# Optimization experiments

Measured on AMD Instinct MI355X. Metric: run time of the kernel, lower is better.

The kernel has to match this reference:

```python
import jax, jax.numpy as jnp
import numpy as np
from jax import lax

DN = ('NCHW', 'OIHW', 'NCHW')
BETA = 0.25


def _conv(x, w, b, stride, pad):
    y = lax.conv_general_dilated(x, w, (stride, stride), [(pad, pad), (pad, pad)],
                                 dimension_numbers=DN)
    return y + b[None, :, None, None]


def _convT(x, w, b, stride, pad, opad):
    # torch ConvTranspose2d(w: [in,out,kh,kw]) == dilated conv with flipped, transposed kernel
    k = w.shape[2]
    wf = jnp.transpose(w, (1, 0, 2, 3))[:, :, ::-1, ::-1]
    lo = k - 1 - pad
    hi = k - 1 - pad + opad
    y = lax.conv_general_dilated(x, wf, (1, 1), [(lo, hi), (lo, hi)],
                                 lhs_dilation=(stride, stride), dimension_numbers=DN)
    return y + b[None, :, None, None]


def setup_inputs() -> dict:
    key = jax.random.key(0)
    ks = jax.random.split(key, 16)
    s = 0.05
    inp = {
        'x': jax.random.normal(ks[0], (64, 3, 125, 125), jnp.float32),
        'enc_w1': jax.random.normal(ks[1], (32, 3, 3, 3), jnp.float32) * s,
        'enc_b1': jnp.zeros((32,), jnp.float32),
        'enc_w2': jax.random.normal(ks[2], (64, 32, 3, 3), jnp.float32) * s,
        'enc_b2': jnp.zeros((64,), jnp.float32),
        'enc_w3': jax.random.normal(ks[3], (64, 64, 1, 1), jnp.float32) * s,
        'enc_b3': jnp.zeros((64,), jnp.float32),
        'codebook': jax.random.normal(ks[4], (512, 64), jnp.float32),
        'dec_w1': jax.random.normal(ks[5], (64, 64, 3, 3), jnp.float32) * s,  # torch [in,out,kh,kw]
        'dec_b1': jnp.zeros((64,), jnp.float32),
        'dec_w2': jax.random.normal(ks[6], (64, 32, 3, 3), jnp.float32) * s,
        'dec_b2': jnp.zeros((32,), jnp.float32),
        'dec_w3': jax.random.normal(ks[7], (32, 3, 2, 2), jnp.float32) * s,
        'dec_b3': jnp.zeros((3,), jnp.float32),
    }
    return inp


def reference(x, enc_w1, enc_b1, enc_w2, enc_b2, enc_w3, enc_b3, codebook,
              dec_w1, dec_b1, dec_w2, dec_b2, dec_w3, dec_b3):
    # Encoder
    z = jax.nn.relu(_conv(x, enc_w1, enc_b1, 2, 1))
    z = jax.nn.relu(_conv(z, enc_w2, enc_b2, 2, 1))
    z = _conv(z, enc_w3, enc_b3, 1, 0)  # [B, D, h, w]

    # VQ (training mode)
    zp = jnp.transpose(z, (0, 2, 3, 1))  # [B, h, w, D]
    flat = zp.reshape(-1, zp.shape[-1])  # [N, D]
    d = (jnp.sum(flat * flat, axis=1, keepdims=True)
         + jnp.sum(codebook * codebook, axis=1)
         - 2.0 * flat @ codebook.T)  # [N, K]
    idx = jnp.argmin(d, axis=1)
    q = codebook[idx].reshape(zp.shape)

    q_latent_loss = jnp.mean((q - lax.stop_gradient(zp)) ** 2)
    e_latent_loss = jnp.mean((zp - lax.stop_gradient(q)) ** 2)
    e_q_loss = q_latent_loss + BETA * e_latent_loss

    q_st = zp + lax.stop_gradient(q - zp)  # straight-through
    e = jnp.transpose(q_st, (0, 3, 1, 2))

    # Decoder
    h = jax.nn.relu(_convT(e, dec_w1, dec_b1, 2, 1, 1))
    h = jax.nn.relu(_convT(h, dec_w2, dec_b2, 2, 1, 1))
    x_recon = _convT(h, dec_w3, dec_b3, 1, 2, 0)

    recon_loss = jnp.sum((x_recon - x) ** 2)
    loss_sum = e_q_loss + recon_loss
    return (loss_sum, e_q_loss, recon_loss, x_recon)
```

## Files before the change

kernel.cpp:

```cpp
#include <hip/hip_runtime.h>

#define DEV __device__ __forceinline__
typedef unsigned short u16;
typedef __bf16 bf16x8 __attribute__((ext_vector_type(8)));
typedef float f32x4 __attribute__((ext_vector_type(4)));

DEV u16 f2bf(float f) {
  unsigned u = __float_as_uint(f);
  u += 0x7FFF + ((u >> 16) & 1);
  return (u16)(u >> 16);
}


__global__ __launch_bounds__(256) void k_prep(
    const float* __restrict__ ew1, const float* __restrict__ ew2,
    const float* __restrict__ ew3, const float* __restrict__ dw1,
    const float* __restrict__ dw2, const float* __restrict__ dw3,
    const float* __restrict__ cb,
    float* __restrict__ wc1p, float* __restrict__ wc3p,
    u16* __restrict__ w3f, float* __restrict__ c2,
    u16* __restrict__ w2f, u16* __restrict__ wt1f, u16* __restrict__ wt2f,
    u16* __restrict__ cbf) {
  int i = blockIdx.x * 256 + threadIdx.x;
  if (i < 864) {
    int cl = i & 7; int t = i >> 3; int tap = t % 9; t /= 9; int ci = t % 3; int cog = t / 3;
    wc1p[i] = ew1[((cog * 8 + cl) * 3 + ci) * 9 + tap];
  } else if (i < 4960) {
    int j = i - 864; int cl = j & 7; int t = j >> 3; int ci = t & 63; int cog = t >> 6;
    wc3p[j] = ew3[(cog * 8 + cl) * 64 + ci];
  } else if (i < 9056) {
    int j = i - 4960;
    int jj = j & 7; int lane = (j >> 3) & 63; int tp = (j >> 9) & 3; int hl = j >> 11;
    int kh = tp >> 1, kw = tp & 1;
    int ci = ((lane >> 4) << 3) + jj; int co = lane & 15;
    float wv = (co < 3) ? dw3[((ci * 3 + co) * 2 + kh) * 2 + kw] : 0.f;
    u16 hi = f2bf(wv);
    if (hl == 0) w3f[j] = hi;
    else         w3f[j] = f2bf(wv - __uint_as_float((unsigned)hi << 16));
  } else if (i < 9568) {
    int k = i - 9056;
    const float4* c4 = (const float4*)(cb + (k << 6));
    float s = 0.f;
    #pragma unroll
    for (int q = 0; q < 16; ++q) { float4 v = c4[q]; s += v.x*v.x + v.y*v.y + v.z*v.z + v.w*v.w; }
    c2[k] = s;
  } else if (i < 28000) {
    int j = i - 9568;
    int jj = j & 7; int lane = (j >> 3) & 63; int nf = (j >> 9) & 3; int kt = j >> 11;
    int kh = kt / 3, kw = kt % 3;
    int ci = ((lane >> 4) << 3) + jj; int co = (nf << 4) + (lane & 15);
    w2f[j] = f2bf(ew2[((co * 32 + ci) * 3 + kh) * 3 + kw]);
  } else if (i < 64864) {
    int j = i - 28000;
    int jj = j & 7; int lane = (j >> 3) & 63; int nf = (j >> 9) & 3; int s = (j >> 11) & 1; int kt = j >> 12;
    int kh = kt / 3, kw = kt % 3;
    int ci = (s << 5) + ((lane >> 4) << 3) + jj; int co = (nf << 4) + (lane & 15);
    wt1f[j] = f2bf(dw1[((ci * 64 + co) * 3 + kh) * 3 + kw]);
  } else if (i < 83296) {
    int j = i - 64864;
    int jj = j & 7; int lane = (j >> 3) & 63; int nf = (j >> 9) & 1; int s = (j >> 10) & 1; int kt = j >> 11;
    int kh = kt / 3, kw = kt % 3;
    int ci = (s << 5) + ((lane >> 4) << 3) + jj; int co = (nf << 4) + (lane & 15);
    wt2f[j] = f2bf(dw2[((ci * 32 + co) * 3 + kh) * 3 + kw]);
  } else if (i < 148832) {
    int j = i - 83296;
    int jj = j & 7; int lane = (j >> 3) & 63; int nt = (j >> 9) & 31; int ks = (j >> 14) & 1; int hl = j >> 15;
    int ci = (ks << 5) + ((lane >> 4) << 3) + jj;
    int code = (nt << 4) + (lane & 15);
    float v = cb[(code << 6) + ci];
    u16 hi = f2bf(v);
    cbf[j] = hl ? f2bf(v - __uint_as_float((unsigned)hi << 16)) : hi;
  }
}

__global__ __launch_bounds__(256) void k_pad(
    const float* __restrict__ x, float* __restrict__ xp) {
  int idx = blockIdx.x * 256 + threadIdx.x;
  int c4 = idx & 31;
  int r  = (idx >> 5) % 129;
  int cbp = (idx >> 5) / 129;
  int ih = r - 1;
  float4 v = make_float4(0.f, 0.f, 0.f, 0.f);
  if ((unsigned)ih < 125u) {
    const float* rp = x + (cbp * 125 + ih) * 125;
    int iw0 = c4 * 4 - 1;
    if (iw0 >= 0)        v.x = rp[iw0];
    if (iw0 + 1 < 125)   v.y = rp[iw0 + 1];
    if (iw0 + 2 < 125)   v.z = rp[iw0 + 2];
    if (iw0 + 3 < 125)   v.w = rp[iw0 + 3];
  }
  *(float4*)(xp + (cbp * 129 + r) * 128 + c4 * 4) = v;
}

__global__ __launch_bounds__(256) void k_conv1(
    const float* __restrict__ xp, const float* __restrict__ wp,
    const float* __restrict__ bias, u16* __restrict__ z1t) {
  __shared__ u16 st[256 * 34];
  int t = threadIdx.x;
  int slab = blockIdx.x & 15, b = blockIdx.x >> 4;
  int tx = t & 15, ty = (t >> 4) & 3, cg = t >> 6;
  int oh = slab * 4 + ty;
  int co0 = cg * 8;
  const float* wcg = wp + cg * 216;
  float acc[8][4];
  #pragma unroll
  for (int c = 0; c < 8; ++c) {
    float bv = bias[co0 + c];
    #pragma unroll
    for (int s = 0; s < 4; ++s) acc[c][s] = bv;
  }
  #pragma unroll
  for (int ci = 0; ci < 3; ++ci) {
    #pragma unroll
    for (int kh = 0; kh < 3; ++kh) {
      const float* rp = xp + ((b * 3 + ci) * 129 + (2 * oh + kh)) * 128 + 8 * tx;
      float4 qa = *(const float4*)rp;
      float4 qb = *(const float4*)(rp + 4);
      float v8 = rp[8];
      float v[9] = {qa.x, qa.y, qa.z, qa.w, qb.x, qb.y, qb.z, qb.w, v8};
      #pragma unroll
      for (int kw = 0; kw < 3; ++kw) {
        const float* wq = wcg + (ci * 9 + kh * 3 + kw) * 8;
        float4 wa = *(const float4*)wq;
        float4 wb = *(const float4*)(wq + 4);
        float w8[8] = {wa.x, wa.y, wa.z, wa.w, wb.x, wb.y, wb.z, wb.w};
        #pragma unroll
        for (int s = 0; s < 4; ++s) {
          float in = v[2 * s + kw];
          #pragma unroll
          for (int c = 0; c < 8; ++c) acc[c][s] = fmaf(in, w8[c], acc[c][s]);
        }
      }
    }
  }
  #pragma unroll
  for (int s = 0; s < 4; ++s) {
    bool wok = (tx * 4 + s) < 63;
    unsigned p0 = 0, p1 = 0, p2 = 0, p3 = 0;
    if (wok) {
      p0 = f2bf(fmaxf(acc[0][s], 0.f)) | ((unsigned)f2bf(fmaxf(acc[1][s], 0.f)) << 16);
      p1 = f2bf(fmaxf(acc[2][s], 0.f)) | ((unsigned)f2bf(fmaxf(acc[3][s], 0.f)) << 16);
      p2 = f2bf(fmaxf(acc[4][s], 0.f)) | ((unsigned)f2bf(fmaxf(acc[5][s], 0.f)) << 16);
      p3 = f2bf(fmaxf(acc[6][s], 0.f)) | ((unsigned)f2bf(fmaxf(acc[7][s], 0.f)) << 16);
    }
    int lpix = tx * 16 + ty * 4 + s;
    *(uint4*)&st[lpix * 34 + co0] = make_uint4(p0, p1, p2, p3);
// ... 145 lines not shown
    #pragma unroll
    for (int r = 0; r < 4; ++r) { bs[mt][r] = 3.4e38f; bix[mt][r] = 0; }
  for (int nt = 0; nt < 32; ++nt) {
    const u16* bp = cbf + lane * 8;
    bf16x8 Bh0 = *(const bf16x8*)(bp + (nt << 9));
    bf16x8 Bh1 = *(const bf16x8*)(bp + ((32 + nt) << 9));
    bf16x8 Bl0 = *(const bf16x8*)(bp + ((64 + nt) << 9));
    bf16x8 Bl1 = *(const bf16x8*)(bp + ((96 + nt) << 9));
    float c2 = c2v[(nt << 4) + n];
    #pragma unroll
    for (int mt = 0; mt < 4; ++mt) {
      f32x4 acc = {0.f, 0.f, 0.f, 0.f};
      acc = __builtin_amdgcn_mfma_f32_16x16x32_bf16(Ah[mt][0], Bh0, acc, 0, 0, 0);
      acc = __builtin_amdgcn_mfma_f32_16x16x32_bf16(Ah[mt][1], Bh1, acc, 0, 0, 0);
      acc = __builtin_amdgcn_mfma_f32_16x16x32_bf16(Al[mt][0], Bh0, acc, 0, 0, 0);
      acc = __builtin_amdgcn_mfma_f32_16x16x32_bf16(Al[mt][1], Bh1, acc, 0, 0, 0);
      acc = __builtin_amdgcn_mfma_f32_16x16x32_bf16(Ah[mt][0], Bl0, acc, 0, 0, 0);
      acc = __builtin_amdgcn_mfma_f32_16x16x32_bf16(Ah[mt][1], Bl1, acc, 0, 0, 0);
      int idx = (nt << 4) + n;
      #pragma unroll
      for (int r = 0; r < 4; ++r) {
        float sc = fmaf(-2.f, acc[r], c2);
        if (sc < bs[mt][r]) { bs[mt][r] = sc; bix[mt][r] = idx; }
      }
    }
  }
  #pragma unroll
  for (int off = 8; off > 0; off >>= 1) {
    #pragma unroll
    for (int mt = 0; mt < 4; ++mt)
      #pragma unroll
      for (int r = 0; r < 4; ++r) {
        float os = __shfl_xor(bs[mt][r], off, 16);
        int oi = __shfl_xor(bix[mt][r], off, 16);
        if (os < bs[mt][r] || (os == bs[mt][r] && oi < bix[mt][r])) {
          bs[mt][r] = os; bix[mt][r] = oi;
        }
      }
  }
  if (n == 0) {
    #pragma unroll
    for (int mt = 0; mt < 4; ++mt)
      #pragma unroll
      for (int r = 0; r < 4; ++r)
        idxb[p0 + mt * 16 + q * 4 + r] = bix[mt][r];
  }
}

__global__ __launch_bounds__(256) void k_vqf(
    const float* __restrict__ z3, const float* __restrict__ cb,
    const int* __restrict__ idxb, u16* __restrict__ et,
    float* __restrict__ acc) {
  int n = blockIdx.x * 256 + threadIdx.x;
  int bi = idxb[n];
  int b = n >> 10, hw = n & 1023;
  const float* zp = z3 + (b << 16) + hw;
  uint2* ep = (uint2*)(et + (n << 6));
  const float4* cq = (const float4*)(cb + (bi << 6));
  float lsum = 0.f;
  #pragma unroll
  for (int i = 0; i < 16; ++i) {
    float4 c = cq[i];
    float zv, df;
    zv = zp[(4*i+0) << 10]; df = c.x - zv; lsum = fmaf(df, df, lsum);
    zv = zp[(4*i+1) << 10]; df = c.y - zv; lsum = fmaf(df, df, lsum);
    zv = zp[(4*i+2) << 10]; df = c.z - zv; lsum = fmaf(df, df, lsum);
    zv = zp[(4*i+3) << 10]; df = c.w - zv; lsum = fmaf(df, df, lsum);
    ep[i] = make_uint2(f2bf(c.x) | ((unsigned)f2bf(c.y) << 16),
                       f2bf(c.z) | ((unsigned)f2bf(c.w) << 16));
  }
  __shared__ float red[256];
  red[threadIdx.x] = lsum; __syncthreads();
  #pragma unroll
  for (int s = 128; s > 0; s >>= 1) {
    if (threadIdx.x < s) red[threadIdx.x] += red[threadIdx.x + s];
    __syncthreads();
  }
  if (threadIdx.x == 0) atomicAdd(acc + 0, red[0]);
}

__global__ __launch_bounds__(256) void k_convT1(
    const u16* __restrict__ et, const u16* __restrict__ wf,
    const float* __restrict__ bias, u16* __restrict__ h1t) {
  __shared__ u16 st[2][64 * 66];
  int t = threadIdx.x;
  int lane = t & 63, wv = t >> 6;
  int n = lane & 15, q = lane >> 4;
  int y = blockIdx.x & 31, b = blockIdx.x >> 5;
  int cog = wv >> 1, xt = wv & 1;
  int m = xt * 16 + n;
  const u16* base0 = et + (((b * 32 + y) * 32) << 6) + q * 8;
  bf16x8 P00a, P00b, P01a = {}, P01b = {}, P10a = {}, P10b = {}, P11a = {}, P11b = {};
  { const u16* p = base0 + (m << 6); P00a = *(const bf16x8*)p; P00b = *(const bf16x8*)(p + 32); }
  if (m + 1 < 32) { const u16* p = base0 + ((m + 1) << 6); P01a = *(const bf16x8*)p; P01b = *(const bf16x8*)(p + 32); }
  if (y + 1 < 32) {
    const u16* base1 = base0 + (32 << 6);
    { const u16* p = base1 + (m << 6); P10a = *(const bf16x8*)p; P10b = *(const bf16x8*)(p + 32); }
    if (m + 1 < 32) { const u16* p = base1 + ((m + 1) << 6); P11a = *(const bf16x8*)p; P11b = *(const bf16x8*)(p + 32); }
  }
  f32x4 accE[2][2] = {};
  f32x4 accO[2][2] = {};
  #pragma unroll
  for (int kw = 0; kw < 3; ++kw) {
    int pwi = (kw == 1) ? 0 : 1;
    bf16x8 A0a = (kw == 0) ? P01a : P00a;
    bf16x8 A0b = (kw == 0) ? P01b : P00b;
    bf16x8 A1a = (kw == 0) ? P11a : P10a;
    bf16x8 A1b = (kw == 0) ? P11b : P10b;
    const u16* wbE = wf + ((3 + kw) << 12) + lane * 8;
    const u16* wbO0 = wf + (kw << 12) + lane * 8;
    const u16* wbO2 = wf + ((6 + kw) << 12) + lane * 8;
    #pragma unroll
    for (int j = 0; j < 2; ++j) {
      int nf = cog * 2 + j;
      bf16x8 bE0 = *(const bf16x8*)(wbE + nf * 512);
      bf16x8 bE1 = *(const bf16x8*)(wbE + (4 + nf) * 512);
      accE[j][pwi] = __builtin_amdgcn_mfma_f32_16x16x32_bf16(A0a, bE0, accE[j][pwi], 0, 0, 0);
      accE[j][pwi] = __builtin_amdgcn_mfma_f32_16x16x32_bf16(A0b, bE1, accE[j][pwi], 0, 0, 0);
      bf16x8 bO00 = *(const bf16x8*)(wbO0 + nf * 512);
      bf16x8 bO01 = *(const bf16x8*)(wbO0 + (4 + nf) * 512);
      accO[j][pwi] = __builtin_amdgcn_mfma_f32_16x16x32_bf16(A1a, bO00, accO[j][pwi], 0, 0, 0);
      accO[j][pwi] = __builtin_amdgcn_mfma_f32_16x16x32_bf16(A1b, bO01, accO[j][pwi], 0, 0, 0);
      bf16x8 bO20 = *(const bf16x8*)(wbO2 + nf * 512);
      bf16x8 bO21 = *(const bf16x8*)(wbO2 + (4 + nf) * 512);
      accO[j][pwi] = __builtin_amdgcn_mfma_f32_16x16x32_bf16(A0a, bO20, accO[j][pwi], 0, 0, 0);
      accO[j][pwi] = __builtin_amdgcn_mfma_f32_16x16x32_bf16(A0b, bO21, accO[j][pwi], 0, 0, 0);
    }
  }
  #pragma unroll
  for (int j = 0; j < 2; ++j) {
    int co = (cog * 2 + j) * 16 + n;
    float bv = bias[co];
    #pragma unroll
    for (int pw = 0; pw < 2; ++pw)
      #pragma unroll
      for (int r = 0; r < 4; ++r) {
        int ow = 2 * (xt * 16 + q * 4 + r) + pw;
        st[0][ow * 66 + co] = f2bf(fmaxf(accE[j][pw][r] + bv, 0.f));
        st[1][ow * 66 + co] = f2bf(fmaxf(accO[j][pw][r] + bv, 0.f));
      }
  }
  __syncthreads();
  int ow = t >> 2, sg = t & 3;
  #pragma unroll
  for (int l = 0; l < 2; ++l) {
    const u16* lp = &st[l][ow * 66 + sg * 16];
    unsigned w0 = *(const unsigned*)(lp + 0), w1 = *(const unsigned*)(lp + 2);
    unsigned w2 = *(const unsigned*)(lp + 4), w3 = *(const unsigned*)(lp + 6);
    unsigned w4 = *(const unsigned*)(lp + 8), w5 = *(const unsigned*)(lp + 10);
    unsigned w6 = *(const unsigned*)(lp + 12), w7 = *(const unsigned*)(lp + 14);
    uint4* gp = (uint4*)(h1t + (((b * 64 + 2 * y + l) * 64 + ow) << 6) + sg * 16);
    gp[0] = make_uint4(w0, w1, w2, w3);
    gp[1] = make_uint4(w4, w5, w6, w7);
  }
}

__global__ __launch_bounds__(256) void k_convT2(
    const u16* __restrict__ h1t, const u16* __restrict__ wf,
    const float* __restrict__ bias, u16* __restrict__ h2t) {
  __shared__ u16 st[2][128 * 34];
  int t = threadIdx.x;
  int lane = t & 63, xt = t >> 6;
  int n = lane & 15, q = lane >> 4;
  int y = blockIdx.x & 63, b = blockIdx.x >> 6;
  int m = xt * 16 + n;
  const u16* base0 = h1t + (((b * 64 + y) * 64) << 6) + q * 8;
  bf16x8 P00a, P00b, P01a = {}, P01b = {}, P10a = {}, P10b = {}, P11a = {}, P11b = {};
  { const u16* p = base0 + (m << 6); P00a = *(const bf16x8*)p; P00b = *(const bf16x8*)(p + 32); }
  if (m + 1 < 64) { const u16* p = base0 + ((m + 1) << 6); P01a = *(const bf16x8*)p; P01b = *(const bf16x8*)(p + 32); }
  if (y + 1 < 64) {
    const u16* base1 = base0 + (64 << 6);
    { const u16* p = base1 + (m << 6); P10a = *(const bf16x8*)p; P10b = *(const bf16x8*)(p + 32); }
    if (m + 1 < 64) { const u16* p = base1 + ((m + 1) << 6); P11a = *(const bf16x8*)p; P11b = *(const bf16x8*)(p + 32); }
  }
  f32x4 accE[2][2] = {};
  f32x4 accO[2][2] = {};
  #pragma unroll
  for (int kw = 0; kw < 3; ++kw) {
    int pwi = (kw == 1) ? 0 : 1;
    bf16x8 A0a = (kw == 0) ? P01a : P00a;
    bf16x8 A0b = (kw == 0) ? P01b : P00b;
    bf16x8 A1a = (kw == 0) ? P11a : P10a;
    bf16x8 A1b = (kw == 0) ? P11b : P10b;
    const u16* wbE = wf + ((3 + kw) << 11) + lane * 8;
    const u16* wbO0 = wf + (kw << 11) + lane * 8;
    const u16* wbO2 = wf + ((6 + kw) << 11) + lane * 8;
    #pragma unroll
    for (int nf = 0; nf < 2; ++nf) {
      bf16x8 bE0 = *(const bf16x8*)(wbE + nf * 512);
      bf16x8 bE1 = *(const bf16x8*)(wbE + (2 + nf) * 512);
      accE[nf][pwi] = __builtin_amdgcn_mfma_f32_16x16x32_bf16(A0a, bE0, accE[nf][pwi], 0, 0, 0);
      accE[nf][pwi] = __builtin_amdgcn_mfma_f32_16x16x32_bf16(A0b, bE1, accE[nf][pwi], 0, 0, 0);
      bf16x8 bO00 = *(const bf16x8*)(wbO0 + nf * 512);
      bf16x8 bO01 = *(const bf16x8*)(wbO0 + (2 + nf) * 512);
      accO[nf][pwi] = __builtin_amdgcn_mfma_f32_16x16x32_bf16(A1a, bO00, accO[nf][pwi], 0, 0, 0);
      accO[nf][pwi] = __builtin_amdgcn_mfma_f32_16x16x32_bf16(A1b, bO01, accO[nf][pwi], 0, 0, 0);
      bf16x8 bO20 = *(const bf16x8*)(wbO2 + nf * 512);
      bf16x8 bO21 = *(const bf16x8*)(wbO2 + (2 + nf) * 512);
      accO[nf][pwi] = __builtin_amdgcn_mfma_f32_16x16x32_bf16(A0a, bO20, accO[nf][pwi], 0, 0, 0);
      accO[nf][pwi] = __builtin_amdgcn_mfma_f32_16x16x32_bf16(A0b, bO21, accO[nf][pwi], 0, 0, 0);
    }
  }
  #pragma unroll
  for (int nf = 0; nf < 2; ++nf) {
    int co = nf * 16 + n;
    float bv = bias[co];
    #pragma unroll
    for (int pw = 0; pw < 2; ++pw)
      #pragma unroll
      for (int r = 0; r < 4; ++r) {
        int ow = 2 * (xt * 16 + q * 4 + r) + pw;
        st[0][ow * 34 + co] = f2bf(fmaxf(accE[nf][pw][r] + bv, 0.f));
        st[1][ow * 34 + co] = f2bf(fmaxf(accO[nf][pw][r] + bv, 0.f));
      }
  }
  __syncthreads();
  int ow = t >> 1, sg = t & 1;
  #pragma unroll
  for (int l = 0; l < 2; ++l) {
    const u16* lp = &st[l][ow * 34 + sg * 16];
    unsigned w0 = *(const unsigned*)(lp + 0), w1 = *(const unsigned*)(lp + 2);
    unsigned w2 = *(const unsigned*)(lp + 4), w3 = *(const unsigned*)(lp + 6);
    unsigned w4 = *(const unsigned*)(lp + 8), w5 = *(const unsigned*)(lp + 10);
    unsigned w6 = *(const unsigned*)(lp + 12), w7 = *(const unsigned*)(lp + 14);
    uint4* gp = (uint4*)(h2t + ((((b * 128 + 2 * y + l) * 128) + ow) << 5) + sg * 16);
    gp[0] = make_uint4(w0, w1, w2, w3);
    gp[1] = make_uint4(w4, w5, w6, w7);
  }
}

__global__ __launch_bounds__(256) void k_convT3(
    const u16* __restrict__ h2t, const u16* __restrict__ w3f,
    const float* __restrict__ bias, const float* __restrict__ x,
    float* __restrict__ xr, float* __restrict__ psum) {
  int t = threadIdx.x;
  int lane = t & 63, wv = t >> 6;
  int n = lane & 15, q = lane >> 4;
  int oh = blockIdx.x % 125, b = blockIdx.x / 125;
  const u16* wbp = w3f + lane * 8;
  bf16x8 Bh0 = *(const bf16x8*)(wbp);
  bf16x8 Bh1 = *(const bf16x8*)(wbp + 512);
  bf16x8 Bh2 = *(const bf16x8*)(wbp + 1024);
  bf16x8 Bh3 = *(const bf16x8*)(wbp + 1536);
  bf16x8 Bl0 = *(const bf16x8*)(wbp + 2048);
  bf16x8 Bl1 = *(const bf16x8*)(wbp + 2560);
  bf16x8 Bl2 = *(const bf16x8*)(wbp + 3072);
  bf16x8 Bl3 = *(const bf16x8*)(wbp + 3584);
  const u16* row1 = h2t + (((long)b * 128 + (oh + 1)) << 7) * 32 + q * 8;
  const u16* row2 = row1 + 4096;
  float bv = (n < 3) ? bias[n] : 0.f;
  float lsum = 0.f;
  #pragma unroll
  for (int ti = 0; ti < 2; ++ti) {
    int tt = wv + ti * 4;
    int c1 = tt * 16 + n + 1;
    int c2 = c1 + 1;
    bf16x8 a11 = {}, a12 = {}, a21 = {}, a22 = {};
    if (c1 < 128) { a11 = *(const bf16x8*)(row1 + (c1 << 5));
                    a21 = *(const bf16x8*)(row2 + (c1 << 5)); }
    if (c2 < 128) { a12 = *(const bf16x8*)(row1 + (c2 << 5));
                    a22 = *(const bf16x8*)(row2 + (c2 << 5)); }
    f32x4 acc = {0.f, 0.f, 0.f, 0.f};
    acc = __builtin_amdgcn_mfma_f32_16x16x32_bf16(a11, Bh3, acc, 0, 0, 0);
    acc = __builtin_amdgcn_mfma_f32_16x16x32_bf16(a12, Bh2, acc, 0, 0, 0);
    acc = __builtin_amdgcn_mfma_f32_16x16x32_bf16(a21, Bh1, acc, 0, 0, 0);
    acc = __builtin_amdgcn_mfma_f32_16x16x32_bf16(a22, Bh0, acc, 0, 0, 0);
    acc = __builtin_amdgcn_mfma_f32_16x16x32_bf16(a11, Bl3, acc, 0, 0, 0);
    acc = __builtin_amdgcn_mfma_f32_16x16x32_bf16(a12, Bl2, acc, 0, 0, 0);
    acc = __builtin_amdgcn_mfma_f32_16x16x32_bf16(a21, Bl1, acc, 0, 0, 0);
    acc = __builtin_amdgcn_mfma_f32_16x16x32_bf16(a22, Bl0, acc, 0, 0, 0);
    if (n < 3) {
      int ow0 = tt * 16 + q * 4;
      int o = b * 46875 + n * 15625 + oh * 125 + ow0;
      if (ow0 + 3 < 125) {
        float4 v = make_float4(acc[0] + bv, acc[1] + bv, acc[2] + bv, acc[3] + bv);
        float4 xv = *(const float4*)(x + o);
        *(float4*)(xr + o) = v;
        float d0 = v.x - xv.x, d1 = v.y - xv.y, d2 = v.z - xv.z, d3 = v.w - xv.w;
        lsum += d0 * d0 + d1 * d1 + d2 * d2 + d3 * d3;
      } else {
        #pragma unroll
        for (int r = 0; r < 4; ++r) {
          if (ow0 + r < 125) {
            float v = acc[r] + bv;
            xr[o + r] = v;
            float d = v - x[o + r];
            lsum = fmaf(d, d, lsum);
          }
        }
      }
    }
  }
  __shared__ float red[256];
  red[t] = lsum; __syncthreads();
  #pragma unroll
  for (int s = 128; s > 0; s >>= 1) {
    if (t < s) red[t] += red[t + s];
    __syncthreads();
  }
  if (t == 0) psum[blockIdx.x] = red[0];
}

__global__ __launch_bounds__(256) void k_fin(
    const float* __restrict__ acc, const float* __restrict__ psum,
    float* __restrict__ out) {
  int t = threadIdx.x;
  float s = 0.f;
  for (int i = t; i < 8000; i += 256) s += psum[i];
  __shared__ float red[256];
  red[t] = s; __syncthreads();
  #pragma unroll
  for (int k = 128; k > 0; k >>= 1) {
    if (t < k) red[t] += red[t + k];
    __syncthreads();
  }
  if (t == 0) {
    float eq  = 1.25f * acc[0] / 4194304.0f;
    float rec = red[0];
    out[0] = eq + rec;
    out[1] = eq;
    out[2] = rec;
  }
}

extern "C" void kernel_launch(void* const* d_in, const int* in_sizes, int n_in,
                              void* d_out, int out_size, void* d_ws, size_t ws_size,
                              hipStream_t stream) {
  (void)in_sizes; (void)n_in; (void)out_size; (void)ws_size;
  const float* x   = (const float*)d_in[0];
  const float* ew1 = (const float*)d_in[1];
  const float* eb1 = (const float*)d_in[2];
  const float* ew2 = (const float*)d_in[3];
  const float* eb2 = (const float*)d_in[4];
  const float* ew3 = (const float*)d_in[5];
  const float* eb3 = (const float*)d_in[6];
  const float* cb  = (const float*)d_in[7];
  const float* dw1 = (const float*)d_in[8];
  const float* db1 = (const float*)d_in[9];
  const float* dw2 = (const float*)d_in[10];
  const float* db2 = (const float*)d_in[11];
  const float* dw3 = (const float*)d_in[12];
  const float* db3 = (const float*)d_in[13];
  float* out = (float*)d_out;
  char*  ws  = (char*)d_ws;

  float*  acc  = (float*)(ws + 0);
  float*  c2   = (float*)(ws + 256);
  float*  wc1p = (float*)(ws + 4096);
  float*  wc3p = (float*)(ws + 8192);
  u16*    w3f  = (u16*)  (ws + 24576);
  u16*    w2f  = (u16*)  (ws + 36864);
  u16*    wt1f = (u16*)  (ws + 73728);
  u16*    wt2f = (u16*)  (ws + 147456);
  float*  psum = (float*)(ws + 184320);
  u16*    cbf  = (u16*)  (ws + 262144);
  u16*    z1t  = (u16*)  (ws + 1048576);
  float*  z2   = (float*)(ws + 18874368);
  float*  z3   = (float*)(ws + 35651584);
  int*    idxb = (int*)  (ws + 52428800);
  u16*    et   = (u16*)  (ws + 54525952);
  u16*    h1t  = (u16*)  (ws + 1048576);
  u16*    h2t  = (u16*)  (ws + 67108864);
  u16*    z3h  = (u16*)  (ws + 134217728);
  u16*    z3l  = (u16*)  (ws + 142606336);
  float*  xp   = (float*)(ws + 150994944);

  hipMemsetAsync(acc, 0, 64, stream);
  k_prep  <<<582,  256, 0, stream>>>(ew1, ew2, ew3, dw1, dw2, dw3, cb,
                                     wc1p, wc3p, w3f, c2, w2f, wt1f, wt2f, cbf);
  k_pad   <<<3096, 256, 0, stream>>>(x, xp);
  k_conv1 <<<1024, 256, 0, stream>>>(xp, wc1p, eb1, z1t);
  k_conv2 <<<2048, 256, 0, stream>>>(z1t, w2f, eb2, z2);
  k_conv3 <<<512,  256, 0, stream>>>(z2, wc3p, eb3, z3, z3h, z3l);
  k_vqp   <<<256,  256, 0, stream>>>(z3h, z3l, cbf, c2, idxb);
  k_vqf   <<<256,  256, 0, stream>>>(z3, cb, idxb, et, acc);
  k_convT1<<<2048, 256, 0, stream>>>(et, wt1f, db1, h1t);
  k_convT2<<<4096, 256, 0, stream>>>(h1t, wt2f, db2, h2t);
  k_convT3<<<8000, 256, 0, stream>>>(h2t, w3f, db3, x, out + 3, psum);
  k_fin   <<<1,    256, 0, stream>>>(acc, psum, out);
}
```

Before: 314.8 us.

## Switch transposed-conv kernels to 32x32x16 MFMA with two rows per block

The two stride-2 transposed-convolution decoder kernels now use 32x32x16 bf16 MFMA tiles instead of 16x16x32, with the weight pre-packing reordered to match the new fragment layout. Each block now computes two input rows (four output rows), which halves the grid size. The staging through shared memory writes whole 128-byte channel rows to global memory. The aim is fewer MFMA issues, fewer B-fragment loads per output and wider stores, at the cost of more live registers for the larger accumulators and A fragments.

```diff
diff --git a/kernel.cpp b/kernel.cpp
--- a/kernel.cpp
+++ b/kernel.cpp
@@ -4,6 +4,7 @@
 typedef unsigned short u16;
 typedef __bf16 bf16x8 __attribute__((ext_vector_type(8)));
 typedef float f32x4 __attribute__((ext_vector_type(4)));
+typedef float f32x16 __attribute__((ext_vector_type(16)));
 
 DEV u16 f2bf(float f) {
   unsigned u = __float_as_uint(f);
@@ -19,7 +20,7 @@
     const float* __restrict__ cb,
     float* __restrict__ wc1p, float* __restrict__ wc3p,
     u16* __restrict__ w3f, float* __restrict__ c2,
-    u16* __restrict__ w2f, u16* __restrict__ wt1f, u16* __restrict__ wt2f,
+    u16* __restrict__ w2f, u16* __restrict__ wt1g, u16* __restrict__ wt2g,
     u16* __restrict__ cbf) {
   int i = blockIdx.x * 256 + threadIdx.x;
   if (i < 864) {
@@ -52,16 +53,16 @@
     w2f[j] = f2bf(ew2[((co * 32 + ci) * 3 + kh) * 3 + kw]);
   } else if (i < 64864) {
     int j = i - 28000;
-    int jj = j & 7; int lane = (j >> 3) & 63; int nf = (j >> 9) & 3; int s = (j >> 11) & 1; int kt = j >> 12;
-    int kh = kt / 3, kw = kt % 3;
-    int ci = (s << 5) + ((lane >> 4) << 3) + jj; int co = (nf << 4) + (lane & 15);
-    wt1f[j] = f2bf(dw1[((ci * 64 + co) * 3 + kh) * 3 + kw]);
+    int jj = j & 7; int lane = (j >> 3) & 63; int cg = (j >> 9) & 1; int s = (j >> 10) & 3; int kt = j >> 12;
+    int ci = s * 16 + ((lane >> 5) << 3) + jj;
+    int co = cg * 32 + (lane & 31);
+    wt1g[j] = f2bf(dw1[(ci * 64 + co) * 9 + kt]);
   } else if (i < 83296) {
     int j = i - 64864;
-    int jj = j & 7; int lane = (j >> 3) & 63; int nf = (j >> 9) & 1; int s = (j >> 10) & 1; int kt = j >> 11;
-    int kh = kt / 3, kw = kt % 3;
-    int ci = (s << 5) + ((lane >> 4) << 3) + jj; int co = (nf << 4) + (lane & 15);
-    wt2f[j] = f2bf(dw2[((ci * 32 + co) * 3 + kh) * 3 + kw]);
+    int jj = j & 7; int lane = (j >> 3) & 63; int s = (j >> 9) & 3; int kt = j >> 11;
+    int ci = s * 16 + ((lane >> 5) << 3) + jj;
+    int co = lane & 31;
+    wt2g[j] = f2bf(dw2[(ci * 32 + co) * 9 + kt]);
   } else if (i < 148832) {
     int j = i - 83296;
     int jj = j & 7; int lane = (j >> 3) & 63; int nt = (j >> 9) & 31; int ks = (j >> 14) & 1; int hl = j >> 15;
@@ -373,150 +374,149 @@
 __global__ __launch_bounds__(256) void k_convT1(
     const u16* __restrict__ et, const u16* __restrict__ wf,
     const float* __restrict__ bias, u16* __restrict__ h1t) {
-  __shared__ u16 st[2][64 * 66];
+  __shared__ u16 st[4][64 * 66];
   int t = threadIdx.x;
   int lane = t & 63, wv = t >> 6;
-  int n = lane & 15, q = lane >> 4;
-  int y = blockIdx.x & 31, b = blockIdx.x >> 5;
-  int cog = wv >> 1, xt = wv & 1;
-  int m = xt * 16 + n;
-  const u16* base0 = et + (((b * 32 + y) * 32) << 6) + q * 8;
-  bf16x8 P00a, P00b, P01a = {}, P01b = {}, P10a = {}, P10b = {}, P11a = {}, P11b = {};
-  { const u16* p = base0 + (m << 6); P00a = *(const bf16x8*)p; P00b = *(const bf16x8*)(p + 32); }
-  if (m + 1 < 32) { const u16* p = base0 + ((m + 1) << 6); P01a = *(const bf16x8*)p; P01b = *(const bf16x8*)(p + 32); }
-  if (y + 1 < 32) {
-    const u16* base1 = base0 + (32 << 6);
-    { const u16* p = base1 + (m << 6); P10a = *(const bf16x8*)p; P10b = *(const bf16x8*)(p + 32); }
-    if (m + 1 < 32) { const u16* p = base1 + ((m + 1) << 6); P11a = *(const bf16x8*)p; P11b = *(const bf16x8*)(p + 32); }
-  }
-  f32x4 accE[2][2] = {};
-  f32x4 accO[2][2] = {};
+  int yw = wv & 1, cog = wv >> 1;
+  int yg = blockIdx.x & 15, b = blockIdx.x >> 4;
+  int y = yg * 2 + yw;
+  int ml = lane & 31, half = lane >> 5;
+  int co = cog * 32 + ml;
+  float bv = bias[co];
+  bf16x8 A[2][2][4];
+  #pragma unroll
+  for (int r = 0; r < 2; ++r)
+    #pragma unroll
+    for (int sh = 0; sh < 2; ++sh)
+      #pragma unroll
+      for (int s = 0; s < 4; ++s) A[r][sh][s] = bf16x8{};
+  {
+    const u16* base = et + (((b * 32 + y) * 32) << 6) + half * 8;
+    #pragma unroll
+    for (int s = 0; s < 4; ++s) A[0][0][s] = *(const bf16x8*)(base + (ml << 6) + s * 16);
+    if (ml + 1 < 32) {
+      #pragma unroll
+      for (int s = 0; s < 4; ++s) A[0][1][s] = *(const bf16x8*)(base + ((ml + 1) << 6) + s * 16);
+    }
+    if (y + 1 < 32) {
+      const u16* base1 = base + (32 << 6);
+      #pragma unroll
+      for (int s = 0; s < 4; ++s) A[1][0][s] = *(const bf16x8*)(base1 + (ml << 6) + s * 16);
+      if (ml + 1 < 32) {
+        #pragma unroll
+        for (int s = 0; s < 4; ++s) A[1][1][s] = *(const bf16x8*)(base1 + ((ml + 1) << 6) + s * 16);
+      }
+    }
+  }
+  f32x16 accE[2] = {}, accO[2] = {};
   #pragma unroll
   for (int kw = 0; kw < 3; ++kw) {
     int pwi = (kw == 1) ? 0 : 1;
-    bf16x8 A0a = (kw == 0) ? P01a : P00a;
-    bf16x8 A0b = (kw == 0) ? P01b : P00b;
-    bf16x8 A1a = (kw == 0) ? P11a : P10a;
-    bf16x8 A1b = (kw == 0) ? P11b : P10b;
-    const u16* wbE = wf + ((3 + kw) << 12) + lane * 8;
-    const u16* wbO0 = wf + (kw << 12) + lane * 8;
-    const u16* wbO2 = wf + ((6 + kw) << 12) + lane * 8;
-    #pragma unroll
-    for (int j = 0; j < 2; ++j) {
-      int nf = cog * 2 + j;
-      bf16x8 bE0 = *(const bf16x8*)(wbE + nf * 512);
-      bf16x8 bE1 = *(const bf16x8*)(wbE + (4 + nf) * 512);
-      accE[j][pwi] = __builtin_amdgcn_mfma_f32_16x16x32_bf16(A0a, bE0, accE[j][pwi], 0, 0, 0);
-      accE[j][pwi] = __builtin_amdgcn_mfma_f32_16x16x32_bf16(A0b, bE1, accE[j][pwi], 0, 0, 0);
-      bf16x8 bO00 = *(const bf16x8*)(wbO0 + nf * 512);
-      bf16x8 bO01 = *(const bf16x8*)(wbO0 + (4 + nf) * 512);
-      accO[j][pwi] = __builtin_amdgcn_mfma_f32_16x16x32_bf16(A1a, bO00, accO[j][pwi], 0, 0, 0);
-      accO[j][pwi] = __builtin_amdgcn_mfma_f32_16x16x32_bf16(A1b, bO01, accO[j][pwi], 0, 0, 0);
-      bf16x8 bO20 = *(const bf16x8*)(wbO2 + nf * 512);
-      bf16x8 bO21 = *(const bf16x8*)(wbO2 + (4 + nf) * 512);
-      accO[j][pwi] = __builtin_amdgcn_mfma_f32_16x16x32_bf16(A0a, bO20, accO[j][pwi], 0, 0, 0);
-      accO[j][pwi] = __builtin_amdgcn_mfma_f32_16x16x32_bf16(A0b, bO21, accO[j][pwi], 0, 0, 0);
-    }
-  }
-  #pragma unroll
-  for (int j = 0; j < 2; ++j) {
-    int co = (cog * 2 + j) * 16 + n;
-    float bv = bias[co];
-    #pragma unroll
-    for (int pw = 0; pw < 2; ++pw)
-      #pragma unroll
-      for (int r = 0; r < 4; ++r) {
-        int ow = 2 * (xt * 16 + q * 4 + r) + pw;
-        st[0][ow * 66 + co] = f2bf(fmaxf(accE[j][pw][r] + bv, 0.f));
-        st[1][ow * 66 + co] = f2bf(fmaxf(accO[j][pw][r] + bv, 0.f));
-      }
-  }
+    int sh = (kw == 0) ? 1 : 0;
+    #pragma unroll
+    for (int s = 0; s < 4; ++s) {
+      bf16x8 a0 = A[0][sh][s], a1 = A[1][sh][s];
+      const u16* wE  = wf + ((((3 + kw) << 2) + s) << 10) + (cog << 9) + lane * 8;
+      const u16* wO0 = wf + (((kw << 2) + s) << 10) + (cog << 9) + lane * 8;
+      const u16* wO2 = wf + ((((6 + kw) << 2) + s) << 10) + (cog << 9) + lane * 8;
+      accE[pwi] = __builtin_amdgcn_mfma_f32_32x32x16_bf16(a0, *(const bf16x8*)wE,  accE[pwi], 0, 0, 0);
+      accO[pwi] = __builtin_amdgcn_mfma_f32_32x32x16_bf16(a1, *(const bf16x8*)wO0, accO[pwi], 0, 0, 0);
+      accO[pwi] = __builtin_amdgcn_mfma_f32_32x32x16_bf16(a0, *(const bf16x8*)wO2, accO[pwi], 0, 0, 0);
+    }
+  }
+  #pragma unroll
+  for (int pw = 0; pw < 2; ++pw)
+    #pragma unroll
+    for (int reg = 0; reg < 16; ++reg) {
+      int m_l = (reg & 3) + ((reg >> 2) << 3) + (half << 2);
+      int ow = 2 * m_l + pw;
+      st[yw * 2 + 0][ow * 66 + co] = f2bf(fmaxf(accE[pw][reg] + bv, 0.f));
+      st[yw * 2 + 1][ow * 66 + co] = f2bf(fmaxf(accO[pw][reg] + bv, 0.f));
+    }
   __syncthreads();
-  int ow = t >> 2, sg = t & 3;
-  #pragma unroll
-  for (int l = 0; l < 2; ++l) {
-    const u16* lp = &st[l][ow * 66 + sg * 16];
-    unsigned w0 = *(const unsigned*)(lp + 0), w1 = *(const unsigned*)(lp + 2);
-    unsigned w2 = *(const unsigned*)(lp + 4), w3 = *(const unsigned*)(lp + 6);
-    unsigned w4 = *(const unsigned*)(lp + 8), w5 = *(const unsigned*)(lp + 10);
-    unsigned w6 = *(const unsigned*)(lp + 12), w7 = *(const unsigned*)(lp + 14);
-    uint4* gp = (uint4*)(h1t + (((b * 64 + 2 * y + l) * 64 + ow) << 6) + sg * 16);
-    gp[0] = make_uint4(w0, w1, w2, w3);
-    gp[1] = make_uint4(w4, w5, w6, w7);
+  {
+    int row = t >> 6, ow = t & 63;
+    const u16* lp = &st[row][ow * 66];
+    uint4* gp = (uint4*)(h1t + (((b * 64 + yg * 4 + row) * 64 + ow) << 6));
+    #pragma unroll
+    for (int g = 0; g < 8; ++g) gp[g] = *(const uint4*)(lp + g * 8);
   }
 }
 
 __global__ __launch_bounds__(256) void k_convT2(
     const u16* __restrict__ h1t, const u16* __restrict__ wf,
     const float* __restrict__ bias, u16* __restrict__ h2t) {
-  __shared__ u16 st[2][128 * 34];
-  int t = threadIdx.x;
-  int lane = t & 63, xt = t >> 6;
-  int n = lane & 15, q = lane >> 4;
-  int y = blockIdx.x & 63, b = blockIdx.x >> 6;
-  int m = xt * 16 + n;
-  const u16* base0 = h1t + (((b * 64 + y) * 64) << 6) + q * 8;
-  bf16x8 P00a, P00b, P01a = {}, P01b = {}, P10a = {}, P10b = {}, P11a = {}, P11b = {};
-  { const u16* p = base0 + (m << 6); P00a = *(const bf16x8*)p; P00b = *(const bf16x8*)(p + 32); }
-  if (m + 1 < 64) { const u16* p = base0 + ((m + 1) << 6); P01a = *(const bf16x8*)p; P01b = *(const bf16x8*)(p + 32); }
-  if (y + 1 < 64) {
-    const u16* base1 = base0 + (64 << 6);
-    { const u16* p = base1 + (m << 6); P10a = *(const bf16x8*)p; P10b = *(const bf16x8*)(p + 32); }
-    if (m + 1 < 64) { const u16* p = base1 + ((m + 1) << 6); P11a = *(const bf16x8*)p; P11b = *(const bf16x8*)(p + 32); }
-  }
-  f32x4 accE[2][2] = {};
-  f32x4 accO[2][2] = {};
+  __shared__ u16 st[4][128 * 34];
+  int t = threadIdx.x;
+  int lane = t & 63, wv = t >> 6;
+  int yw = wv & 1, xt = wv >> 1;
+  int yg = blockIdx.x & 31, b = blockIdx.x >> 5;
+  int y = yg * 2 + yw;
+  int ml = lane & 31, half = lane >> 5;
+  int m = xt * 32 + ml;
+  int co = ml;
+  float bv = bias[co];
+  bf16x8 A[2][2][4];
+  #pragma unroll
+  for (int r = 0; r < 2; ++r)
+    #pragma unroll
+    for (int sh = 0; sh < 2; ++sh)
+      #pragma unroll
+      for (int s = 0; s < 4; ++s) A[r][sh][s] = bf16x8{};
+  {
+    const u16* base = h1t + (((b * 64 + y) * 64) << 6) + half * 8;
+    #pragma unroll
+    for (int s = 0; s < 4; ++s) A[0][0][s] = *(const bf16x8*)(base + (m << 6) + s * 16);
+    if (m + 1 < 64) {
+      #pragma unroll
+      for (int s = 0; s < 4; ++s) A[0][1][s] = *(const bf16x8*)(base + ((m + 1) << 6) + s * 16);
+    }
+    if (y + 1 < 64) {
+      const u16* base1 = base + (64 << 6);
+      #pragma unroll
+      for (int s = 0; s < 4; ++s) A[1][0][s] = *(const bf16x8*)(base1 + (m << 6) + s * 16);
+      if (m + 1 < 64) {
+        #pragma unroll
+        for (int s = 0; s < 4; ++s) A[1][1][s] = *(const bf16x8*)(base1 + ((m + 1) << 6) + s * 16);
+      }
+    }
+  }
+  f32x16 accE[2] = {}, accO[2] = {};
   #pragma unroll
   for (int kw = 0; kw < 3; ++kw) {
     int pwi = (kw == 1) ? 0 : 1;
-    bf16x8 A0a = (kw == 0) ? P01a : P00a;
-    bf16x8 A0b = (kw == 0) ? P01b : P00b;
-    bf16x8 A1a = (kw == 0) ? P11a : P10a;
-    bf16x8 A1b = (kw == 0) ? P11b : P10b;
-    const u16* wbE = wf + ((3 + kw) << 11) + lane * 8;
-    const u16* wbO0 = wf + (kw << 11) + lane * 8;
-    const u16* wbO2 = wf + ((6 + kw) << 11) + lane * 8;
-    #pragma unroll
-    for (int nf = 0; nf < 2; ++nf) {
-      bf16x8 bE0 = *(const bf16x8*)(wbE + nf * 512);
-      bf16x8 bE1 = *(const bf16x8*)(wbE + (2 + nf) * 512);
-      accE[nf][pwi] = __builtin_amdgcn_mfma_f32_16x16x32_bf16(A0a, bE0, accE[nf][pwi], 0, 0, 0);
-      accE[nf][pwi] = __builtin_amdgcn_mfma_f32_16x16x32_bf16(A0b, bE1, accE[nf][pwi], 0, 0, 0);
-      bf16x8 bO00 = *(const bf16x8*)(wbO0 + nf * 512);
-      bf16x8 bO01 = *(const bf16x8*)(wbO0 + (2 + nf) * 512);
-      accO[nf][pwi] = __builtin_amdgcn_mfma_f32_16x16x32_bf16(A1a, bO00, accO[nf][pwi], 0, 0, 0);
-      accO[nf][pwi] = __builtin_amdgcn_mfma_f32_16x16x32_bf16(A1b, bO01, accO[nf][pwi], 0, 0, 0);
-      bf16x8 bO20 = *(const bf16x8*)(wbO2 + nf * 512);
-      bf16x8 bO21 = *(const bf16x8*)(wbO2 + (2 + nf) * 512);
-      accO[nf][pwi] = __builtin_amdgcn_mfma_f32_16x16x32_bf16(A0a, bO20, accO[nf][pwi], 0, 0, 0);
-      accO[nf][pwi] = __builtin_amdgcn_mfma_f32_16x16x32_bf16(A0b, bO21, accO[nf][pwi], 0, 0, 0);
-    }
-  }
-  #pragma unroll
-  for (int nf = 0; nf < 2; ++nf) {
-    int co = nf * 16 + n;
-    float bv = bias[co];
-    #pragma unroll
-    for (int pw = 0; pw < 2; ++pw)
-      #pragma unroll
-      for (int r = 0; r < 4; ++r) {
-        int ow = 2 * (xt * 16 + q * 4 + r) + pw;
-        st[0][ow * 34 + co] = f2bf(fmaxf(accE[nf][pw][r] + bv, 0.f));
-        st[1][ow * 34 + co] = f2bf(fmaxf(accO[nf][pw][r] + bv, 0.f));
-      }
-  }
+    int sh = (kw == 0) ? 1 : 0;
+    #pragma unroll
+    for (int s = 0; s < 4; ++s) {
+      bf16x8 a0 = A[0][sh][s], a1 = A[1][sh][s];
+      const u16* wE  = wf + ((((3 + kw) << 2) + s) << 9) + lane * 8;
+      const u16* wO0 = wf + (((kw << 2) + s) << 9) + lane * 8;
+      const u16* wO2 = wf + ((((6 + kw) << 2) + s) << 9) + lane * 8;
+      accE[pwi] = __builtin_amdgcn_mfma_f32_32x32x16_bf16(a0, *(const bf16x8*)wE,  accE[pwi], 0, 0, 0);
+      accO[pwi] = __builtin_amdgcn_mfma_f32_32x32x16_bf16(a1, *(const bf16x8*)wO0, accO[pwi], 0, 0, 0);
+      accO[pwi] = __builtin_amdgcn_mfma_f32_32x32x16_bf16(a0, *(const bf16x8*)wO2, accO[pwi], 0, 0, 0);
+    }
+  }
+  #pragma unroll
+  for (int pw = 0; pw < 2; ++pw)
+    #pragma unroll
+    for (int reg = 0; reg < 16; ++reg) {
+      int m_l = (reg & 3) + ((reg >> 2) << 3) + (half << 2);
+      int ow = 2 * (xt * 32 + m_l) + pw;
+      st[yw * 2 + 0][ow * 34 + co] = f2bf(fmaxf(accE[pw][reg] + bv, 0.f));
+      st[yw * 2 + 1][ow * 34 + co] = f2bf(fmaxf(accO[pw][reg] + bv, 0.f));
+    }
   __syncthreads();
-  int ow = t >> 1, sg = t & 1;
-  #pragma unroll
-  for (int l = 0; l < 2; ++l) {
-    const u16* lp = &st[l][ow * 34 + sg * 16];
-    unsigned w0 = *(const unsigned*)(lp + 0), w1 = *(const unsigned*)(lp + 2);
-    unsigned w2 = *(const unsigned*)(lp + 4), w3 = *(const unsigned*)(lp + 6);
-    unsigned w4 = *(const unsigned*)(lp + 8), w5 = *(const unsigned*)(lp + 10);
-    unsigned w6 = *(const unsigned*)(lp + 12), w7 = *(const unsigned*)(lp + 14);
-    uint4* gp = (uint4*)(h2t + ((((b * 128 + 2 * y + l) * 128) + ow) << 5) + sg * 16);
-    gp[0] = make_uint4(w0, w1, w2, w3);
-    gp[1] = make_uint4(w4, w5, w6, w7);
+  #pragma unroll
+  for (int l2 = 0; l2 < 2; ++l2) {
+    int idx = t * 2 + l2;
+    int row = idx >> 7, ow = idx & 127;
+    const u16* lp = &st[row][ow * 34];
+    uint4* gp = (uint4*)(h2t + (((b * 128 + yg * 4 + row) * 128 + ow) << 5));
+    gp[0] = *(const uint4*)(lp);
+    gp[1] = *(const uint4*)(lp + 8);
+    gp[2] = *(const uint4*)(lp + 16);
+    gp[3] = *(const uint4*)(lp + 24);
   }
 }
 
@@ -641,8 +641,8 @@
   float*  wc3p = (float*)(ws + 8192);
   u16*    w3f  = (u16*)  (ws + 24576);
   u16*    w2f  = (u16*)  (ws + 36864);
-  u16*    wt1f = (u16*)  (ws + 73728);
-  u16*    wt2f = (u16*)  (ws + 147456);
+  u16*    wt1g = (u16*)  (ws + 73728);
+  u16*    wt2g = (u16*)  (ws + 147456);
   float*  psum = (float*)(ws + 184320);
   u16*    cbf  = (u16*)  (ws + 262144);
   u16*    z1t  = (u16*)  (ws + 1048576);
@@ -658,15 +658,15 @@
 
   hipMemsetAsync(acc, 0, 64, stream);
   k_prep  <<<582,  256, 0, stream>>>(ew1, ew2, ew3, dw1, dw2, dw3, cb,
-                                     wc1p, wc3p, w3f, c2, w2f, wt1f, wt2f, cbf);
+                                     wc1p, wc3p, w3f, c2, w2f, wt1g, wt2g, cbf);
   k_pad   <<<3096, 256, 0, stream>>>(x, xp);
   k_conv1 <<<1024, 256, 0, stream>>>(xp, wc1p, eb1, z1t);
   k_conv2 <<<2048, 256, 0, stream>>>(z1t, w2f, eb2, z2);
   k_conv3 <<<512,  256, 0, stream>>>(z2, wc3p, eb3, z3, z3h, z3l);
   k_vqp   <<<256,  256, 0, stream>>>(z3h, z3l, cbf, c2, idxb);
   k_vqf   <<<256,  256, 0, stream>>>(z3, cb, idxb, et, acc);
-  k_convT1<<<2048, 256, 0, stream>>>(et, wt1f, db1, h1t);
-  k_convT2<<<4096, 256, 0, stream>>>(h1t, wt2f, db2, h2t);
+  k_convT1<<<1024, 256, 0, stream>>>(et, wt1g, db1, h1t);
+  k_convT2<<<2048, 256, 0, stream>>>(h1t, wt2g, db2, h2t);
   k_convT3<<<8000, 256, 0, stream>>>(h2t, w3f, db3, x, out + 3, psum);
   k_fin   <<<1,    256, 0, stream>>>(acc, psum, out);
 }
```

Measured after the change: 325.3 us. 1.03x slower.

## Stage transposed-conv weights in LDS and retile convT1 blocks by channel half

Applied to the files above, without the earlier changes.

Both decoder transposed-conv kernels now copy their bf16 weight fragments into shared memory once per block, then read B operands from LDS instead of global/L2 on every MFMA step. convT1 is retiled so each block handles one half of the output channels across two input rows, so each block stages only its half of the weights. Its output staging buffer becomes four rows of 32 channels, written back as contiguous 64-byte chunks. This adds about 36 KB of LDS per block and an extra barrier, which may lower occupancy. It also doubles redundant activation loads across the two channel-half blocks.

```diff
diff --git a/kernel.cpp b/kernel.cpp
--- a/kernel.cpp
+++ b/kernel.cpp
@@ -373,12 +373,28 @@
 __global__ __launch_bounds__(256) void k_convT1(
     const u16* __restrict__ et, const u16* __restrict__ wf,
     const float* __restrict__ bias, u16* __restrict__ h1t) {
-  __shared__ u16 st[2][64 * 66];
+  __shared__ u16 wl[36 * 512];
+  __shared__ u16 st[4][64 * 34];
   int t = threadIdx.x;
   int lane = t & 63, wv = t >> 6;
+  int yw = wv & 1, xt = wv >> 1;
+  int cog = blockIdx.x & 1;
+  int yg = (blockIdx.x >> 1) & 15;
+  int b = blockIdx.x >> 5;
+  {
+    const uint4* gw = (const uint4*)wf;
+    uint4* lw = (uint4*)wl;
+    #pragma unroll
+    for (int k = 0; k < 9; ++k) {
+      int i = t + 256 * k;
+      int slot = i >> 6, within = i & 63;
+      int kt = slot >> 2, j = (slot >> 1) & 1, ks = slot & 1;
+      int goff = (kt << 12) + (((ks << 2) + (cog << 1) + j) << 9);
+      lw[i] = gw[(goff >> 3) + within];
+    }
+  }
+  int y = yg * 2 + yw;
   int n = lane & 15, q = lane >> 4;
-  int y = blockIdx.x & 31, b = blockIdx.x >> 5;
-  int cog = wv >> 1, xt = wv & 1;
   int m = xt * 16 + n;
   const u16* base0 = et + (((b * 32 + y) * 32) << 6) + q * 8;
   bf16x8 P00a, P00b, P01a = {}, P01b = {}, P10a = {}, P10b = {}, P11a = {}, P11b = {};
@@ -389,6 +405,7 @@
     { const u16* p = base1 + (m << 6); P10a = *(const bf16x8*)p; P10b = *(const bf16x8*)(p + 32); }
     if (m + 1 < 32) { const u16* p = base1 + ((m + 1) << 6); P11a = *(const bf16x8*)p; P11b = *(const bf16x8*)(p + 32); }
   }
+  __syncthreads();
   f32x4 accE[2][2] = {};
   f32x4 accO[2][2] = {};
   #pragma unroll
@@ -398,62 +415,65 @@
     bf16x8 A0b = (kw == 0) ? P01b : P00b;
     bf16x8 A1a = (kw == 0) ? P11a : P10a;
     bf16x8 A1b = (kw == 0) ? P11b : P10b;
-    const u16* wbE = wf + ((3 + kw) << 12) + lane * 8;
-    const u16* wbO0 = wf + (kw << 12) + lane * 8;
-    const u16* wbO2 = wf + ((6 + kw) << 12) + lane * 8;
     #pragma unroll
     for (int j = 0; j < 2; ++j) {
-      int nf = cog * 2 + j;
-      bf16x8 bE0 = *(const bf16x8*)(wbE + nf * 512);
-      bf16x8 bE1 = *(const bf16x8*)(wbE + (4 + nf) * 512);
+      const u16* wE  = wl + ((((3 + kw) << 2) + (j << 1)) << 9) + lane * 8;
+      const u16* wO0 = wl + (((kw << 2) + (j << 1)) << 9) + lane * 8;
+      const u16* wO2 = wl + ((((6 + kw) << 2) + (j << 1)) << 9) + lane * 8;
+      bf16x8 bE0 = *(const bf16x8*)wE;
+      bf16x8 bE1 = *(const bf16x8*)(wE + 512);
       accE[j][pwi] = __builtin_amdgcn_mfma_f32_16x16x32_bf16(A0a, bE0, accE[j][pwi], 0, 0, 0);
       accE[j][pwi] = __builtin_amdgcn_mfma_f32_16x16x32_bf16(A0b, bE1, accE[j][pwi], 0, 0, 0);
-      bf16x8 bO00 = *(const bf16x8*)(wbO0 + nf * 512);
-      bf16x8 bO01 = *(const bf16x8*)(wbO0 + (4 + nf) * 512);
+      bf16x8 bO00 = *(const bf16x8*)wO0;
+      bf16x8 bO01 = *(const bf16x8*)(wO0 + 512);
       accO[j][pwi] = __builtin_amdgcn_mfma_f32_16x16x32_bf16(A1a, bO00, accO[j][pwi], 0, 0, 0);
       accO[j][pwi] = __builtin_amdgcn_mfma_f32_16x16x32_bf16(A1b, bO01, accO[j][pwi], 0, 0, 0);
-      bf16x8 bO20 = *(const bf16x8*)(wbO2 + nf * 512);
-      bf16x8 bO21 = *(const bf16x8*)(wbO2 + (4 + nf) * 512);
+      bf16x8 bO20 = *(const bf16x8*)wO2;
+      bf16x8 bO21 = *(const bf16x8*)(wO2 + 512);
       accO[j][pwi] = __builtin_amdgcn_mfma_f32_16x16x32_bf16(A0a, bO20, accO[j][pwi], 0, 0, 0);
       accO[j][pwi] = __builtin_amdgcn_mfma_f32_16x16x32_bf16(A0b, bO21, accO[j][pwi], 0, 0, 0);
     }
   }
   #pragma unroll
   for (int j = 0; j < 2; ++j) {
-    int co = (cog * 2 + j) * 16 + n;
-    float bv = bias[co];
+    int col = j * 16 + n;
+    float bv = bias[cog * 32 + col];
     #pragma unroll
     for (int pw = 0; pw < 2; ++pw)
       #pragma unroll
       for (int r = 0; r < 4; ++r) {
         int ow = 2 * (xt * 16 + q * 4 + r) + pw;
-        st[0][ow * 66 + co] = f2bf(fmaxf(accE[j][pw][r] + bv, 0.f));
-        st[1][ow * 66 + co] = f2bf(fmaxf(accO[j][pw][r] + bv, 0.f));
+        st[yw * 2 + 0][ow * 34 + col] = f2bf(fmaxf(accE[j][pw][r] + bv, 0.f));
+        st[yw * 2 + 1][ow * 34 + col] = f2bf(fmaxf(accO[j][pw][r] + bv, 0.f));
       }
   }
   __syncthreads();
-  int ow = t >> 2, sg = t & 3;
-  #pragma unroll
-  for (int l = 0; l < 2; ++l) {
-    const u16* lp = &st[l][ow * 66 + sg * 16];
-    unsigned w0 = *(const unsigned*)(lp + 0), w1 = *(const unsigned*)(lp + 2);
-    unsigned w2 = *(const unsigned*)(lp + 4), w3 = *(const unsigned*)(lp + 6);
-    unsigned w4 = *(const unsigned*)(lp + 8), w5 = *(const unsigned*)(lp + 10);
-    unsigned w6 = *(const unsigned*)(lp + 12), w7 = *(const unsigned*)(lp + 14);
-    uint4* gp = (uint4*)(h1t + (((b * 64 + 2 * y + l) * 64 + ow) << 6) + sg * 16);
-    gp[0] = make_uint4(w0, w1, w2, w3);
-    gp[1] = make_uint4(w4, w5, w6, w7);
+  {
+    int row = t >> 6, ow = t & 63;
+    const u16* lp = &st[row][ow * 34];
+    uint4* gp = (uint4*)(h1t + (((b * 64 + yg * 4 + row) * 64 + ow) << 6) + cog * 32);
+    gp[0] = *(const uint4*)(lp);
+    gp[1] = *(const uint4*)(lp + 8);
+    gp[2] = *(const uint4*)(lp + 16);
+    gp[3] = *(const uint4*)(lp + 24);
   }
 }
 
 __global__ __launch_bounds__(256) void k_convT2(
     const u16* __restrict__ h1t, const u16* __restrict__ wf,
     const float* __restrict__ bias, u16* __restrict__ h2t) {
+  __shared__ u16 wl[18432];
   __shared__ u16 st[2][128 * 34];
   int t = threadIdx.x;
   int lane = t & 63, xt = t >> 6;
   int n = lane & 15, q = lane >> 4;
   int y = blockIdx.x & 63, b = blockIdx.x >> 6;
+  {
+    const uint4* gw = (const uint4*)wf;
+    uint4* lw = (uint4*)wl;
+    #pragma unroll
+    for (int k = 0; k < 9; ++k) lw[t + 256 * k] = gw[t + 256 * k];
+  }
   int m = xt * 16 + n;
   const u16* base0 = h1t + (((b * 64 + y) * 64) << 6) + q * 8;
   bf16x8 P00a, P00b, P01a = {}, P01b = {}, P10a = {}, P10b = {}, P11a = {}, P11b = {};
@@ -464,6 +484,7 @@
     { const u16* p = base1 + (m << 6); P10a = *(const bf16x8*)p; P10b = *(const bf16x8*)(p + 32); }
     if (m + 1 < 64) { const u16* p = base1 + ((m + 1) << 6); P11a = *(const bf16x8*)p; P11b = *(const bf16x8*)(p + 32); }
   }
+  __syncthreads();
   f32x4 accE[2][2] = {};
   f32x4 accO[2][2] = {};
   #pragma unroll
@@ -473,9 +494,9 @@
     bf16x8 A0b = (kw == 0) ? P01b : P00b;
     bf16x8 A1a = (kw == 0) ? P11a : P10a;
     bf16x8 A1b = (kw == 0) ? P11b : P10b;
-    const u16* wbE = wf + ((3 + kw) << 11) + lane * 8;
-    const u16* wbO0 = wf + (kw << 11) + lane * 8;
-    const u16* wbO2 = wf + ((6 + kw) << 11) + lane * 8;
+    const u16* wbE = wl + ((3 + kw) << 11) + lane * 8;
+    const u16* wbO0 = wl + (kw << 11) + lane * 8;
+    const u16* wbO2 = wl + ((6 + kw) << 11) + lane * 8;
     #pragma unroll
     for (int nf = 0; nf < 2; ++nf) {
       bf16x8 bE0 = *(const bf16x8*)(wbE + nf * 512);
```

Result: faster. 307.0 us (-2.5%).
